# Kernel optimization log

Hardware: AMD Instinct MI355X
Metric: run time of the kernel (lower is better)

## Reference

```python
import jax, jax.numpy as jnp
import numpy as np

S, T, B, E, H, V = 64, 64, 64, 256, 256, 32000
PAD = 0


def _lstm_layer(X, Wih, Whh, b, h0, c0):
    # X: (time, B, in), torch gate order i,f,g,o
    def step(carry, x_t):
        h, c = carry
        z = x_t @ Wih.T + h @ Whh.T + b
        i, f, g, o = jnp.split(z, 4, axis=-1)
        c = jax.nn.sigmoid(f) * c + jax.nn.sigmoid(i) * jnp.tanh(g)
        h = jax.nn.sigmoid(o) * jnp.tanh(c)
        return (h, c), h
    (hT, cT), outs = jax.lax.scan(step, (h0, c0), X)
    return outs, hT, cT


def setup_inputs() -> dict:
    key = jax.random.key(0)
    ks = jax.random.split(key, 20)
    p = lambda k, shape: (jax.random.normal(k, shape, jnp.float32) * 0.05)
    inp = {
        "source_padded": jax.random.randint(ks[0], (S, B), 0, V, jnp.int32),
        "target_padded": jax.random.randint(ks[1], (T, B), 0, V, jnp.int32),
        "src_emb": p(ks[2], (V, E)),
        "tgt_emb": p(ks[3], (V, E)),
        "enc_Wih_f": p(ks[4], (4 * H, E)),
        "enc_Whh_f": p(ks[5], (4 * H, H)),
        "enc_b_f": p(ks[6], (4 * H,)),
        "enc_Wih_b": p(ks[7], (4 * H, E)),
        "enc_Whh_b": p(ks[8], (4 * H, H)),
        "enc_b_b": p(ks[9], (4 * H,)),
        "dec_Wih": p(ks[10], (4 * H, E + H)),
        "dec_Whh": p(ks[11], (4 * H, H)),
        "dec_b": p(ks[12], (4 * H,)),
        "Wh": p(ks[13], (H, 2 * H)),
        "Wc": p(ks[14], (H, 2 * H)),
        "Watt": p(ks[15], (H, 2 * H)),
        "Wcomb": p(ks[16], (H, 3 * H)),
        "Wvocab": p(ks[17], (V, H)),
    }
    return inp


def reference(source_padded, target_padded, src_emb, tgt_emb,
              enc_Wih_f, enc_Whh_f, enc_b_f, enc_Wih_b, enc_Whh_b, enc_b_b,
              dec_Wih, dec_Whh, dec_b, Wh, Wc, Watt, Wcomb, Wvocab):
    X = src_emb[source_padded]                      # (S,B,E)
    h0 = jnp.zeros((B, H), X.dtype)
    c0 = jnp.zeros((B, H), X.dtype)
    # bidirectional encoder (all sequences full length -> pack is identity)
    fwd_out, hf, cf = _lstm_layer(X, enc_Wih_f, enc_Whh_f, enc_b_f, h0, c0)
    bwd_out, hb, cb = _lstm_layer(X[::-1], enc_Wih_b, enc_Whh_b, enc_b_b, h0, c0)
    bwd_out = bwd_out[::-1]
    enc_hiddens = jnp.concatenate([fwd_out, bwd_out], -1).transpose(1, 0, 2)  # (B,S,2H)
    dec_h = jnp.concatenate([hf, hb], -1) @ Wh.T     # h_projection
    dec_c = jnp.concatenate([cf, cb], -1) @ Wc.T     # c_projection
    enc_proj = enc_hiddens @ Watt.T                  # (B,S,H)

    Y = tgt_emb[target_padded[:-1]]                  # (T-1,B,E)

    def dstep(carry, Y_t):
        h, c, o_prev = carry
        x = jnp.concatenate([Y_t, o_prev], -1)       # (B,E+H)
        z = x @ dec_Wih.T + h @ dec_Whh.T + dec_b
        i, f, g, o = jnp.split(z, 4, axis=-1)
        c = jax.nn.sigmoid(f) * c + jax.nn.sigmoid(i) * jnp.tanh(g)
        h = jax.nn.sigmoid(o) * jnp.tanh(c)
        e_t = jnp.einsum('bsh,bh->bs', enc_proj, h)  # attention scores
        alpha = jax.nn.softmax(e_t, axis=-1)         # no pads -> mask is no-op
        a_t = jnp.einsum('bs,bsd->bd', alpha, enc_hiddens)  # context (B,2H)
        O_t = jnp.tanh(jnp.concatenate([a_t, h], -1) @ Wcomb.T)  # dropout=eval
        return (h, c, O_t), O_t

    _, outs = jax.lax.scan(dstep, (dec_h, dec_c, jnp.zeros((B, H), X.dtype)), Y)
    P = jax.nn.log_softmax(outs @ Wvocab.T, axis=-1)          # (T-1,B,V)
    gold = jnp.take_along_axis(P, target_padded[1:][..., None], axis=-1)[..., 0]
    tmask = (target_padded[1:] != PAD).astype(P.dtype)
    return (gold * tmask).sum(axis=0)                          # (B,)
```

## Files before the change

kernel.cpp:

```cpp
#include <hip/hip_runtime.h>
#include <hip/hip_bf16.h>

static constexpr int S = 64, T = 64, B = 64, E = 256, H = 256, V = 32000;
static constexpr int H4 = 4 * H;
static constexpr int NCHUNK = 500;
static constexpr int NROW = (T - 1) * B;
static constexpr int LDP = 264;

typedef short bf16x8 __attribute__((ext_vector_type(8)));
typedef float f32x4 __attribute__((ext_vector_type(4)));
typedef unsigned long long ull;

__device__ __forceinline__ float sigf(float x) { return 1.0f / (1.0f + __expf(-x)); }
__device__ __forceinline__ float tanhfast(float x) { return 1.0f - 2.0f / (__expf(2.0f * x) + 1.0f); }
__device__ __forceinline__ float bflo(uint w) { return __uint_as_float(w << 16); }
__device__ __forceinline__ float bfhi(uint w) { return __uint_as_float(w & 0xffff0000u); }
__device__ __forceinline__ ushort f2bu(float x) {
  return __bfloat16_as_ushort(__float2bfloat16(x));
}

__device__ __forceinline__ void st_u32(uint* p, uint v) {
  __hip_atomic_store(p, v, __ATOMIC_RELAXED, __HIP_MEMORY_SCOPE_AGENT);
}
__device__ __forceinline__ uint ld_u32(const uint* p) {
  return __hip_atomic_load(p, __ATOMIC_RELAXED, __HIP_MEMORY_SCOPE_AGENT);
}

__global__ __launch_bounds__(256) void k_cvt_bf16(const float* __restrict__ src,
                                                  __hip_bfloat16* __restrict__ dst, int n) {
  int i = blockIdx.x * 256 + threadIdx.x;
  if (i < n) dst[i] = __float2bfloat16(src[i]);
}

__global__ __launch_bounds__(256) void k_cvt_slice(const float* __restrict__ src,
                                                   __hip_bfloat16* __restrict__ dst) {
  int n = blockIdx.x, tid = threadIdx.x;
  dst[n * 256 + tid] = __float2bfloat16(src[n * 512 + tid]);
}

__global__ __launch_bounds__(256) void k_gather(const int* __restrict__ idx,
                                                const float* __restrict__ emb,
                                                __hip_bfloat16* __restrict__ dst) {
  int r = blockIdx.x, tid = threadIdx.x;
  dst[r * 256 + tid] = __float2bfloat16(emb[idx[r] * E + tid]);
}

__global__ __launch_bounds__(256) void k_pack4(const float* __restrict__ src,
                                               uint2* __restrict__ dst,
                                               int total, int jshift, int ld, int off) {
  int idx = blockIdx.x * 256 + threadIdx.x;
  if (idx >= total) return;
  int J = 1 << jshift;
  int i = idx >> jshift, j = idx & (J - 1);
  const float* s = src + (size_t)j * ld + off + 4 * i;
  float4 v = *(const float4*)s;
  uint2 o;
  o.x = (uint)f2bu(v.x) | ((uint)f2bu(v.y) << 16);
  o.y = (uint)f2bu(v.z) | ((uint)f2bu(v.w) << 16);
  dst[(size_t)i * J + j] = o;
}

#define MFMA_TILE_BODY(Abase, Wbase, rb, cb)                                     \
  const int tid = threadIdx.x;                                                   \
  const int lane = tid & 63, wid = tid >> 6;                                     \
  const int wr = wid >> 1, wc = wid & 1;                                         \
  const int l15 = lane & 15, l4 = lane >> 4;                                     \
  for (int it = 0; it < 8; it++) {                                               \
    int c = it * 256 + tid;                                                      \
    int row = c >> 5, off = (c & 31) * 8;                                        \
    *(uint4*)&Asl[row * LDP + off] =                                             \
        *(const uint4*)((Abase) + (size_t)((rb) + row) * 256 + off);             \
    *(uint4*)&Bsl[row * LDP + off] =                                             \
        *(const uint4*)((Wbase) + (size_t)((cb) + row) * 256 + off);             \
  }                                                                              \
  __syncthreads();                                                               \
  f32x4 acc[2][2];                                                               \
  for (int m = 0; m < 2; m++)                                                    \
    for (int n = 0; n < 2; n++) acc[m][n] = (f32x4){0.f, 0.f, 0.f, 0.f};         \
  for (int kk = 0; kk < 8; kk++) {                                               \
    int ko = kk * 32 + l4 * 8;                                                   \
    bf16x8 a0 = *(const bf16x8*)&Asl[(wr * 32 + l15) * LDP + ko];                \
    bf16x8 a1 = *(const bf16x8*)&Asl[(wr * 32 + 16 + l15) * LDP + ko];           \
    bf16x8 b0 = *(const bf16x8*)&Bsl[(wc * 32 + l15) * LDP + ko];                \
    bf16x8 b1 = *(const bf16x8*)&Bsl[(wc * 32 + 16 + l15) * LDP + ko];           \
    acc[0][0] = __builtin_amdgcn_mfma_f32_16x16x32_bf16(a0, b0, acc[0][0], 0, 0, 0); \
    acc[0][1] = __builtin_amdgcn_mfma_f32_16x16x32_bf16(a0, b1, acc[0][1], 0, 0, 0); \
    acc[1][0] = __builtin_amdgcn_mfma_f32_16x16x32_bf16(a1, b0, acc[1][0], 0, 0, 0); \
    acc[1][1] = __builtin_amdgcn_mfma_f32_16x16x32_bf16(a1, b1, acc[1][1], 0, 0, 0); \
  }

__global__ __launch_bounds__(256) void k_gemm_bias(
    const __hip_bfloat16* __restrict__ A, const __hip_bfloat16* __restrict__ W,
    const float* __restrict__ bias, float* __restrict__ C, int ldc) {
  __shared__ __align__(16) ushort Asl[64 * LDP];
  __shared__ __align__(16) ushort Bsl[64 * LDP];
  const int cb = blockIdx.x * 64, rb = blockIdx.y * 64;
  MFMA_TILE_BODY((const ushort*)A, (const ushort*)W, rb, cb)
  #pragma unroll
  for (int m = 0; m < 2; m++)
    #pragma unroll
    for (int n = 0; n < 2; n++) {
      int col = cb + wc * 32 + n * 16 + l15;
      float bv = bias[col];
      #pragma unroll
      for (int r = 0; r < 4; r++) {
        int row = rb + wr * 32 + m * 16 + l4 * 4 + r;
        C[(size_t)row * ldc + col] = acc[m][n][r] + bv;
      }
    }
}

__global__ __launch_bounds__(256) void k_encproj_mfma(
    const __hip_bfloat16* __restrict__ fwd_bf, const __hip_bfloat16* __restrict__ bwd_bf,
    const __hip_bfloat16* __restrict__ Watt_bf, __hip_bfloat16* __restrict__ encproj_bf) {
  __shared__ __align__(16) ushort Asl[64 * LDP];
  __shared__ __align__(16) ushort Bsl[64 * LDP];
  const int cb = blockIdx.x * 64, rb = blockIdx.y * 64;
  const int tid = threadIdx.x;
  const int lane = tid & 63, wid = tid >> 6;
  const int wr = wid >> 1, wc = wid & 1;
  const int l15 = lane & 15, l4 = lane >> 4;
  f32x4 acc[2][2];
  #pragma unroll
  for (int m = 0; m < 2; m++)
    #pragma unroll
    for (int n = 0; n < 2; n++) acc[m][n] = (f32x4){0.f, 0.f, 0.f, 0.f};
  for (int kt = 0; kt < 2; kt++) {
    if (kt) __syncthreads();
    for (int it = 0; it < 8; it++) {
      int c = it * 256 + tid;
      int row = c >> 5, off = (c & 31) * 8;
      int r = rb + row, s = r >> 6, bb = r & 63;
      const ushort* arow = (kt == 0)
          ? (const ushort*)fwd_bf + (size_t)(s * 64 + bb) * 256
          : (const ushort*)bwd_bf + (size_t)(s * 64 + bb) * 256;
      *(uint4*)&Asl[row * LDP + off] = *(const uint4*)(arow + off);
      *(uint4*)&Bsl[row * LDP + off] =
          *(const uint4*)((const ushort*)Watt_bf + (size_t)(cb + row) * 512 + kt * 256 + off);
    }
    __syncthreads();
    for (int kk = 0; kk < 8; kk++) {
      int ko = kk * 32 + l4 * 8;
      bf16x8 a0 = *(const bf16x8*)&Asl[(wr * 32 + l15) * LDP + ko];
      bf16x8 a1 = *(const bf16x8*)&Asl[(wr * 32 + 16 + l15) * LDP + ko];
      bf16x8 b0 = *(const bf16x8*)&Bsl[(wc * 32 + l15) * LDP + ko];
      bf16x8 b1 = *(const bf16x8*)&Bsl[(wc * 32 + 16 + l15) * LDP + ko];
      acc[0][0] = __builtin_amdgcn_mfma_f32_16x16x32_bf16(a0, b0, acc[0][0], 0, 0, 0);
      acc[0][1] = __builtin_amdgcn_mfma_f32_16x16x32_bf16(a0, b1, acc[0][1], 0, 0, 0);
      acc[1][0] = __builtin_amdgcn_mfma_f32_16x16x32_bf16(a1, b0, acc[1][0], 0, 0, 0);
      acc[1][1] = __builtin_amdgcn_mfma_f32_16x16x32_bf16(a1, b1, acc[1][1], 0, 0, 0);
    }
  }
  #pragma unroll
  for (int m = 0; m < 2; m++)
    #pragma unroll
    for (int n = 0; n < 2; n++) {
      int col = cb + wc * 32 + n * 16 + l15;
      #pragma unroll
      for (int r = 0; r < 4; r++) {
        int row = rb + wr * 32 + m * 16 + l4 * 4 + r;
        int s = row >> 6, bb = row & 63;
        ((ushort*)encproj_bf)[(size_t)(bb * 64 + s) * 256 + col] = f2bu(acc[m][n][r]);
      }
    }
}

__global__ __launch_bounds__(256) void k_vocab2(
    const __hip_bfloat16* __restrict__ outs_bf, const __hip_bfloat16* __restrict__ Wv,
    const int* __restrict__ tgt, float* __restrict__ part_max,
    float* __restrict__ part_sum, float* __restrict__ gold) {
  __shared__ __align__(16) ushort Asl[64 * LDP];
  __shared__ __align__(16) ushort Bsl[64 * LDP];
  __shared__ int goldcol[64];
  __shared__ float pm[64][2], ps[64][2];
  const int vb = blockIdx.x;
  const int tid = threadIdx.x;
  const int lane = tid & 63, wid = tid >> 6;
  const int wr = wid >> 1, wc = wid & 1;
  const int l15 = lane & 15, l4 = lane >> 4;
  for (int it = 0; it < 8; it++) {
    int c = it * 256 + tid;
    int row = c >> 5, off = (c & 31) * 8;
    *(uint4*)&Bsl[row * LDP + off] =
        *(const uint4*)((const ushort*)Wv + (size_t)(vb * 64 + row) * 256 + off);
  }
  for (int t = 0; t < T - 1; t++) {
    __syncthreads();
    for (int it = 0; it < 8; it++) {
      int c = it * 256 + tid;
      int row = c >> 5, off = (c & 31) * 8;
      *(uint4*)&Asl[row * LDP + off] =
          *(const uint4*)((const ushort*)outs_bf + (size_t)(t * 64 + row) * 256 + off);
    }
    if (tid < 64) goldcol[tid] = tgt[(t + 1) * B + tid];
    __syncthreads();
    f32x4 acc[2][2];
    #pragma unroll
    for (int m = 0; m < 2; m++)
      #pragma unroll
      for (int n = 0; n < 2; n++) acc[m][n] = (f32x4){0.f, 0.f, 0.f, 0.f};
    for (int kk = 0; kk < 8; kk++) {
      int ko = kk * 32 + l4 * 8;
      bf16x8 a0 = *(const bf16x8*)&Asl[(wr * 32 + l15) * LDP + ko];
      bf16x8 a1 = *(const bf16x8*)&Asl[(wr * 32 + 16 + l15) * LDP + ko];
      bf16x8 b0 = *(const bf16x8*)&Bsl[(wc * 32 + l15) * LDP + ko];
      bf16x8 b1 = *(const bf16x8*)&Bsl[(wc * 32 + 16 + l15) * LDP + ko];
      acc[0][0] = __builtin_amdgcn_mfma_f32_16x16x32_bf16(a0, b0, acc[0][0], 0, 0, 0);
      acc[0][1] = __builtin_amdgcn_mfma_f32_16x16x32_bf16(a0, b1, acc[0][1], 0, 0, 0);
      acc[1][0] = __builtin_amdgcn_mfma_f32_16x16x32_bf16(a1, b0, acc[1][0], 0, 0, 0);
      acc[1][1] = __builtin_amdgcn_mfma_f32_16x16x32_bf16(a1, b1, acc[1][1], 0, 0, 0);
    }
    #pragma unroll
    for (int m = 0; m < 2; m++) {
      #pragma unroll
      for (int r = 0; r < 4; r++) {
        int row_local = wr * 32 + m * 16 + l4 * 4 + r;
        int gc = goldcol[row_local];
        #pragma unroll
        for (int n = 0; n < 2; n++) {
          int col = vb * 64 + wc * 32 + n * 16 + l15;
          if (col == gc) gold[t * 64 + row_local] = acc[m][n][r];
        }
        float v = fmaxf(acc[m][0][r], acc[m][1][r]);
        #pragma unroll
        for (int o = 1; o < 16; o <<= 1) v = fmaxf(v, __shfl_xor(v, o));
        float e = __expf(acc[m][0][r] - v) + __expf(acc[m][1][r] - v);
        #pragma unroll
        for (int o = 1; o < 16; o <<= 1) e += __shfl_xor(e, o);
        if (l15 == 0) { pm[row_local][wc] = v; ps[row_local][wc] = e; }
      }
    }
    __syncthreads();
    if (tid < 64) {
      float m0 = pm[tid][0], m1 = pm[tid][1];
      float M = fmaxf(m0, m1);
      float Ss = ps[tid][0] * __expf(m0 - M) + ps[tid][1] * __expf(m1 - M);
      part_max[(size_t)vb * NROW + t * 64 + tid] = M;
      part_sum[(size_t)vb * NROW + t * 64 + tid] = Ss;
    }
  }
}

__global__ __launch_bounds__(256) void k_enc4(
    const float* __restrict__ XwF, const float* __restrict__ XwB,
    const float* __restrict__ WhhF, const float* __restrict__ WhhB,
    uint* __restrict__ Xenc_u32,
    __hip_bfloat16* __restrict__ fwd_bf, __hip_bfloat16* __restrict__ bwd_bf,
    float* __restrict__ Cfin, uint* __restrict__ eflags) {
  __shared__ __align__(16) ushort Wl[128 * 264];
  __shared__ __align__(16) ushort Xa[16 * 264];
  __shared__ float zz[4][8][33];
  __shared__ float hsb[8][32];
  const int id = blockIdx.x;
  const int g = id & 7, kb = id >> 3;
  const int dir = kb >> 3, s = kb & 7;
  const int tid = threadIdx.x;
  const float* Whh = dir ? WhhB : WhhF;
  const float* Xw = dir ? XwB : XwF;
  uint* fl = eflags + (size_t)(g * 2 + dir) * 8 * 32;
  for (int i = tid; i < 128 * 256; i += 256) {
    int c = i >> 8, k2 = i & 255;
    int gate = c >> 5, jj = c & 31;
    Wl[c * 264 + k2] = f2bu(Whh[(size_t)(gate * 256 + s * 32 + jj) * 256 + k2]);
  }
  for (int i = tid; i < 16 * 264; i += 256) Xa[i] = 0;
  const int lane = tid & 63, w = tid >> 6;
  const int l15 = lane & 15, l4 = lane >> 4;
  const int tb = tid >> 5, tjj = tid & 31;
  float c_reg = 0.f;
  __syncthreads();
  for (int st = 0; st < 64; st++) {
    const int ts = dir ? 63 - st : st;
    const int par = st & 1;
    const uint* Xr = Xenc_u32 + (size_t)(par * 2 + dir) * 8192;
    uint* Xo = Xenc_u32 + (size_t)((par ^ 1) * 2 + dir) * 8192;
    for (int i = tid; i < 8 * 128; i += 256) {
      int row = i >> 7, colu = i & 127;
      uint v = ld_u32(Xr + (size_t)(8 * g + row) * 128 + colu);
      *(uint*)&Xa[row * 264 + colu * 2] = v;
    }
    __syncthreads();
    f32x4 a0v = (f32x4){0.f, 0.f, 0.f, 0.f}, a1v = (f32x4){0.f, 0.f, 0.f, 0.f};
    for (int kk = 0; kk < 8; kk++) {
      bf16x8 af = *(const bf16x8*)&Xa[l15 * 264 + kk * 32 + l4 * 8];
      bf16x8 b0 = *(const bf16x8*)&Wl[((2 * w) * 16 + l15) * 264 + kk * 32 + l4 * 8];
      bf16x8 b1 = *(const bf16x8*)&Wl[((2 * w + 1) * 16 + l15) * 264 + kk * 32 + l4 * 8];
      a0v = __builtin_amdgcn_mfma_f32_16x16x32_bf16(af, b0, a0v, 0, 0, 0);
      a1v = __builtin_amdgcn_mfma_f32_16x16x32_bf16(af, b1, a1v, 0, 0, 0);
    }
    if (l4 < 2) {
      #pragma unroll
      for (int r = 0; r < 4; r++) {
        int b = l4 * 4 + r;
        zz[w][b][l15] = a0v[r];
        zz[w][b][16 + l15] = a1v[r];
      }
    }
    __syncthreads();
    {
      int gb = 8 * g + tb, j = 32 * s + tjj;
      const float* xw = Xw + (size_t)(ts * 64 + gb) * 1024;
      float zi = zz[0][tb][tjj] + xw[j];
      float zf = zz[1][tb][tjj] + xw[256 + j];
      float zg = zz[2][tb][tjj] + xw[512 + j];
      float zo = zz[3][tb][tjj] + xw[768 + j];
      float c = sigf(zf) * c_reg + sigf(zi) * tanhfast(zg);
      c_reg = c;
      float h = sigf(zo) * tanhfast(c);
      hsb[tb][tjj] = h;
      ushort hb = f2bu(h);
      if (dir == 0) ((ushort*)fwd_bf)[(size_t)(st * 64 + gb) * 256 + j] = hb;
      else          ((ushort*)bwd_bf)[(size_t)((63 - st) * 64 + gb) * 256 + j] = hb;
    }
    __syncthreads();
    if (tid < 128) {
      int tb2 = tid >> 4, p = tid & 15;
      uint v = (uint)f2bu(hsb[tb2][2 * p]) | ((uint)f2bu(hsb[tb2][2 * p + 1]) << 16);
      st_u32(Xo + (size_t)(8 * g + tb2) * 128 + 16 * s + p, v);
    }
    __syncthreads();
    if (tid == 0) st_u32(&fl[s * 32], (uint)(st + 1));
    if (tid < 8)
      while (ld_u32(&fl[tid * 32]) < (uint)(st + 1)) __builtin_amdgcn_s_sleep(2);
    asm volatile("" ::: "memory");
    __syncthreads();
  }
  Cfin[(size_t)(dir * 64 + 8 * g + tb) * 256 + 32 * s + tjj] = c_reg;
}

__global__ __launch_bounds__(256) void k_dec_init3(
    const __hip_bfloat16* __restrict__ Xenc, const float* __restrict__ Cfin,
    const float* __restrict__ Wh, const float* __restrict__ Wc,
    uint* __restrict__ Xd_u32, float* __restrict__ decc0) {
  int b = blockIdx.x, tid = threadIdx.x;
  __shared__ __align__(16) float ch[512], cc[512];
  __shared__ float hh[256];
  ch[tid]       = __bfloat162float(Xenc[(size_t)(0 * 64 + b) * 256 + tid]);
  ch[256 + tid] = __bfloat162float(Xenc[(size_t)(1 * 64 + b) * 256 + tid]);
  cc[tid]       = Cfin[(size_t)(0 * 64 + b) * 256 + tid];
  cc[256 + tid] = Cfin[(size_t)(1 * 64 + b) * 256 + tid];
  __syncthreads();
  const float* wh = Wh + tid * 512;
  const float* wc = Wc + tid * 512;
  float ah = 0, ac = 0;
  for (int k = 0; k < 512; k += 4) {
    float4 hv = *(const float4*)&ch[k];
    float4 cv = *(const float4*)&cc[k];
    float4 w1 = *(const float4*)&wh[k];
    float4 w2 = *(const float4*)&wc[k];
    ah += hv.x * w1.x + hv.y * w1.y + hv.z * w1.z + hv.w * w1.w;
    ac += cv.x * w2.x + cv.y * w2.y + cv.z * w2.z + cv.w * w2.w;
  }
  decc0[b * 256 + tid] = ac;
  hh[tid] = ah;
  __syncthreads();
  if (tid < 128) {
    uint v = (uint)f2bu(hh[2 * tid]) | ((uint)f2bu(hh[2 * tid + 1]) << 16);
    Xd_u32[(size_t)b * 256 + tid] = v;
    Xd_u32[(size_t)b * 256 + 128 + tid] = 0u;
  }
}

__global__ __launch_bounds__(512) void k_dec5(
    const float* __restrict__ YW, const float* __restrict__ dWih,
    const float* __restrict__ dWhh, const uint2* __restrict__ Wcq,
    const __hip_bfloat16* __restrict__ encproj_bf,
    const __hip_bfloat16* __restrict__ fwd_bf, const __hip_bfloat16* __restrict__ bwd_bf,
    const float* __restrict__ decc0, uint* __restrict__ Xd_u32,
    __hip_bfloat16* __restrict__ outs_bf,
    uint* __restrict__ zflags, uint* __restrict__ aflags) {
  __shared__ __align__(16) char smem[155648];
  const int id = blockIdx.x;
  const int g = id & 7, kb = id >> 3;
  const int tid = threadIdx.x;
  uint* zfl = zflags + (size_t)g * 8 * 32;
  uint* afl = aflags + (size_t)g * 16 * 32;

  if (kb < 8) {
    const int s = kb;
    ushort* Wl = (ushort*)smem;
    ushort* Xa = (ushort*)(smem + 133120);
    float* zslds = (float*)(smem + 149760);
    float* hsb = (float*)(smem + 153856);
    for (int i = tid; i < 128 * 512; i += 512) {
      int c = i >> 9, k2 = i & 511;
      int gate = c >> 5, jj = c & 31;
      int gr = gate * 256 + 32 * s + jj;
      float v = (k2 < 256) ? dWhh[(size_t)gr * 256 + k2]
                           : dWih[(size_t)gr * 512 + 256 + (k2 - 256)];
      Wl[c * 520 + k2] = f2bu(v);
    }
    for (int i = tid; i < 16 * 520; i += 512) Xa[i] = 0;
    const int lane = tid & 63, w = tid >> 6;
    const int l15 = lane & 15, l4 = lane >> 4;
    float c_reg = 0.f;
    if (tid < 256) {
      int b = tid >> 5, jj = tid & 31;
      c_reg = decc0[(size_t)(8 * g + b) * 256 + 32 * s + jj];
    }
    __syncthreads();
    for (int t = 0; t < 63; t++) {
      if (t > 0) {
        if (tid < 8)
          while (ld_u32(&zfl[tid * 32]) < (uint)t) __builtin_amdgcn_s_sleep(2);
        else if (tid >= 64 && tid < 80)
          while (ld_u32(&afl[(tid - 64) * 32]) < (uint)t) __builtin_amdgcn_s_sleep(2);
        asm volatile("" ::: "memory");
        __syncthreads();
      }
      const uint* Xr = Xd_u32 + (size_t)(t & 1) * 16384;
      for (int i = tid; i < 8 * 256; i += 512) {
        int row = i >> 8, colu = i & 255;
        uint v = ld_u32(Xr + (size_t)(8 * g + row) * 256 + colu);
        *(uint*)&Xa[row * 520 + colu * 2] = v;
      }
      __syncthreads();
      f32x4 accv = (f32x4){0.f, 0.f, 0.f, 0.f};
      for (int kk = 0; kk < 16; kk++) {
        bf16x8 af = *(const bf16x8*)&Xa[l15 * 520 + kk * 32 + l4 * 8];
        bf16x8 bf = *(const bf16x8*)&Wl[(w * 16 + l15) * 520 + kk * 32 + l4 * 8];
        accv = __builtin_amdgcn_mfma_f32_16x16x32_bf16(af, bf, accv, 0, 0, 0);
      }
      if (l4 < 2) {
        #pragma unroll
        for (int r = 0; r < 4; r++) {
          int b = l4 * 4 + r;
          zslds[b * 128 + w * 16 + l15] = accv[r];
        }
      }
      __syncthreads();
      if (tid < 256) {
        int b = tid >> 5, jj = tid & 31;
        int gb = 8 * g + b;
        const float* yw = YW + (size_t)(t * 64 + gb) * 1024 + 32 * s + jj;
        float zi = zslds[b * 128 + jj] + yw[0];
        float zf = zslds[b * 128 + 32 + jj] + yw[256];
        float zg = zslds[b * 128 + 64 + jj] + yw[512];
        float zo = zslds[b * 128 + 96 + jj] + yw[768];
        float c = sigf(zf) * c_reg + sigf(zi) * tanhfast(zg);
        c_reg = c;
        hsb[b * 32 + jj] = sigf(zo) * tanhfast(c);
      }
      __syncthreads();
      if (tid < 128) {
        int b = tid >> 4, p = tid & 15;
        uint v = (uint)f2bu(hsb[b * 32 + 2 * p]) | ((uint)f2bu(hsb[b * 32 + 2 * p + 1]) << 16);
        st_u32(Xd_u32 + (size_t)((t & 1) ^ 1) * 16384 + (size_t)(8 * g + b) * 256 + 16 * s + p, v);
      }
      __syncthreads();
      if (tid == 0) st_u32(&zfl[s * 32], (uint)(t + 1));
    }
  } else {
    const int lb = (kb - 8) >> 1, jh = (kb - 8) & 1;
    const int b = 8 * g + lb;
    ushort* ep = (ushort*)smem;
    ushort* eh = (ushort*)(smem + 33792);
    float* hn = (float*)(smem + 100352);
    float* xcomb = (float*)(smem + 101376);
    float* e_l = (float*)(smem + 104448);
    float* alpha_l = (float*)(smem + 104704);
    float* op_l = (float*)(smem + 104960);
    float* Ost = (float*)(smem + 107008);
    for (int i = tid; i < 64 * 256; i += 512) {
      int s2 = i >> 8, k2 = i & 255;
      ep[s2 * 264 + k2] = ((const ushort*)encproj_bf)[(size_t)(b * 64 + s2) * 256 + k2];
    }
    for (int i = tid; i < 64 * 512; i += 512) {
      int s2 = i >> 9, d = i & 511;
      ushort v = (d < 256) ? ((const ushort*)fwd_bf)[(size_t)(s2 * 64 + b) * 256 + d]
                           : ((const ushort*)bwd_bf)[(size_t)(s2 * 64 + b) * 256 + d - 256];
      eh[s2 * 520 + d] = v;
    }
    __syncthreads();
    for (int t = 0; t < 63; t++) {
      if (tid < 8)
        while (ld_u32(&zfl[tid * 32]) < (uint)(t + 1)) __builtin_amdgcn_s_sleep(2);
      asm volatile("" ::: "memory");
      __syncthreads();
      if (tid < 128) {
        uint v = ld_u32(Xd_u32 + (size_t)((t & 1) ^ 1) * 16384 + (size_t)b * 256 + tid);
        hn[2 * tid] = bflo(v);
        hn[2 * tid + 1] = bfhi(v);
      }
      __syncthreads();
      {
        int s2 = tid >> 3, q8 = tid & 7;
        const ushort* pr = ep + s2 * 264 + q8 * 32;
        const float* hq = hn + q8 * 32;
        float a = 0.f;
        #pragma unroll 8
        for (int kk = 0; kk < 32; kk += 2) {
          uint wv = *(const uint*)(pr + kk);
          a += bflo(wv) * hq[kk] + bfhi(wv) * hq[kk + 1];
        }
        a += __shfl_xor(a, 1);
        a += __shfl_xor(a, 2);
        a += __shfl_xor(a, 4);
        if (q8 == 0) e_l[s2] = a;
      }
      __syncthreads();
      if (tid < 64) {
        float e = e_l[tid];
        float mx = e;
        #pragma unroll
        for (int o = 32; o > 0; o >>= 1) mx = fmaxf(mx, __shfl_xor(mx, o));
        float p = __expf(e - mx);
        float ss = p;
        #pragma unroll
        for (int o = 32; o > 0; o >>= 1) ss += __shfl_xor(ss, o);
        alpha_l[tid] = p / ss;
      }
      __syncthreads();
      {
        float a = 0.f;
        const ushort* col = eh + tid;
        #pragma unroll 8
        for (int s2 = 0; s2 < 64; s2++)
          a += alpha_l[s2] * __uint_as_float(((uint)col[s2 * 520]) << 16);
        xcomb[tid] = a;
        if (tid < 256) xcomb[512 + tid] = hn[tid];
      }
      __syncthreads();
      {
        int jl = tid & 127, kq = tid >> 7;
        int j = jh * 128 + jl;
        const uint2* wp = Wcq + (size_t)(kq * 48) * 256 + j;
        const float4* x4 = (const float4*)xcomb + kq * 48;
        float a = 0.f;
        #pragma unroll 6
        for (int ii = 0; ii < 48; ii++) {
          uint2 wv = wp[(size_t)ii * 256];
          float4 xv = x4[ii];
          a += bflo(wv.x) * xv.x + bfhi(wv.x) * xv.y + bflo(wv.y) * xv.z + bfhi(wv.y) * xv.w;
        }
        op_l[kq * 128 + jl] = a;
      }
      __syncthreads();
      if (tid < 128) {
        float sum = op_l[tid] + op_l[128 + tid] + op_l[256 + tid] + op_l[384 + tid];
        float O = tanhfast(sum);
        Ost[tid] = O;
        ((ushort*)outs_bf)[(size_t)(t * 64 + b) * 256 + jh * 128 + tid] = f2bu(O);
      }
      __syncthreads();
      if (tid < 64) {
        uint v = (uint)f2bu(Ost[2 * tid]) | ((uint)f2bu(Ost[2 * tid + 1]) << 16);
        st_u32(Xd_u32 + (size_t)((t & 1) ^ 1) * 16384 + (size_t)b * 256 + 128 + jh * 64 + tid, v);
      }
      __syncthreads();
      if (tid == 0) st_u32(&afl[(lb * 2 + jh) * 32], (uint)(t + 1));
    }
  }
}

__global__ __launch_bounds__(256) void k_final(
    const float* __restrict__ part_max, const float* __restrict__ part_sum,
    const float* __restrict__ gold, const int* __restrict__ tgt,
    float* __restrict__ out) {
  int b = blockIdx.x, tid = threadIdx.x;
  int tq = tid >> 2, q = tid & 3;
  __shared__ float lm[64][4], ls[64][4];
  __shared__ float red[64];
  if (tq < T - 1) {
    int n = tq * B + b;
    float m = -__builtin_inff(), s = 0;
    for (int i = q; i < NCHUNK; i += 4) {
      float pmv = part_max[(size_t)i * NROW + n];
      float psv = part_sum[(size_t)i * NROW + n];
      float M2 = fmaxf(m, pmv);
      s = s * __expf(m - M2) + psv * __expf(pmv - M2);
      m = M2;
    }
    lm[tq][q] = m;
    ls[tq][q] = s;
  }
  __syncthreads();
  if (tid < T - 1) {
    float M = fmaxf(fmaxf(lm[tid][0], lm[tid][1]), fmaxf(lm[tid][2], lm[tid][3]));
    float Ss = ls[tid][0] * __expf(lm[tid][0] - M) + ls[tid][1] * __expf(lm[tid][1] - M) +
               ls[tid][2] * __expf(lm[tid][2] - M) + ls[tid][3] * __expf(lm[tid][3] - M);
    float lse = M + logf(Ss);
    int g = tgt[(tid + 1) * B + b];
    red[tid] = (g != 0) ? (gold[tid * B + b] - lse) : 0.f;
  }
  if (tid == T - 1) red[T - 1] = 0.f;
  __syncthreads();
  if (tid == 0) {
    float s = 0;
    for (int i = 0; i < T - 1; i++) s += red[i];
    out[b] = s;
  }
}

extern "C" void kernel_launch(void* const* d_in, const int* in_sizes, int n_in,
                              void* d_out, int out_size, void* d_ws, size_t ws_size,
                              hipStream_t stream) {
  (void)in_sizes; (void)n_in; (void)out_size; (void)ws_size;
  const int*   src   = (const int*)  d_in[0];
  const int*   tgt   = (const int*)  d_in[1];
  const float* semb  = (const float*)d_in[2];
  const float* temb  = (const float*)d_in[3];
  const float* WihF  = (const float*)d_in[4];
  const float* WhhF  = (const float*)d_in[5];
  const float* bF    = (const float*)d_in[6];
  const float* WihB  = (const float*)d_in[7];
  const float* WhhB  = (const float*)d_in[8];
  const float* bB    = (const float*)d_in[9];
  const float* dWih  = (const float*)d_in[10];
  const float* dWhh  = (const float*)d_in[11];
  const float* db    = (const float*)d_in[12];
  const float* Wh    = (const float*)d_in[13];
  const float* Wc    = (const float*)d_in[14];
  const float* Watt  = (const float*)d_in[15];
  const float* Wcomb = (const float*)d_in[16];
  const float* Wv    = (const float*)d_in[17];
  float* out = (float*)d_out;

  char* wp = (char*)d_ws;
  auto alloc = [&](size_t bytes) -> char* {
    char* p = wp;
    wp += (bytes + 255) & ~(size_t)255;
    return p;
  };
  float* XwF  = (float*)alloc((size_t)S * B * H4 * 4);
  float* XwB  = (float*)alloc((size_t)S * B * H4 * 4);
  float* YW   = (float*)alloc((size_t)(T - 1) * B * H4 * 4);
  __hip_bfloat16* fwd_bf     = (__hip_bfloat16*)alloc((size_t)S * B * H * 2);
  __hip_bfloat16* bwd_bf     = (__hip_bfloat16*)alloc((size_t)S * B * H * 2);
  __hip_bfloat16* encproj_bf = (__hip_bfloat16*)alloc((size_t)B * S * H * 2);
  __hip_bfloat16* Ag         = (__hip_bfloat16*)alloc((size_t)S * B * E * 2);
  __hip_bfloat16* Yg         = (__hip_bfloat16*)alloc((size_t)(T - 1) * B * E * 2);
  __hip_bfloat16* WihF_bf    = (__hip_bfloat16*)alloc((size_t)H4 * E * 2);
  __hip_bfloat16* WihB_bf    = (__hip_bfloat16*)alloc((size_t)H4 * E * 2);
  __hip_bfloat16* dWih_bf    = (__hip_bfloat16*)alloc((size_t)H4 * E * 2);
  __hip_bfloat16* Wv_bf      = (__hip_bfloat16*)alloc((size_t)V * H * 2);
  __hip_bfloat16* Watt_bf    = (__hip_bfloat16*)alloc((size_t)H * 512 * 2);
  __hip_bfloat16* outs_bf    = (__hip_bfloat16*)alloc((size_t)NROW * H * 2);
  uint2* Wcq = (uint2*)alloc((size_t)192 * 256 * 8);
  float* part_max = (float*)alloc((size_t)NCHUNK * NROW * 4);
  float* part_sum = (float*)alloc((size_t)NCHUNK * NROW * 4);
  float* gold     = (float*)alloc((size_t)NROW * 4);
  float* Cfin  = (float*)alloc((size_t)2 * B * H * 4);
  float* decc0 = (float*)alloc((size_t)B * H * 4);
  __hip_bfloat16* Xenc = (__hip_bfloat16*)alloc((size_t)2 * 2 * B * H * 2);
  uint* Xdec = (uint*)alloc((size_t)2 * B * 256 * 4);
  char* stateBase = wp;
  uint* eflags = (uint*)alloc(16 * 8 * 32 * 4);
  uint* zflags = (uint*)alloc(8 * 8 * 32 * 4);
  uint* aflags = (uint*)alloc(8 * 16 * 32 * 4);
  size_t stateBytes = (size_t)(wp - stateBase);
  hipMemsetAsync(stateBase, 0, stateBytes, stream);
  hipMemsetAsync(Xenc, 0, (size_t)2 * 2 * B * H * 2, stream);

  hipLaunchKernelGGL(k_cvt_bf16, dim3((H4 * E + 255) / 256), dim3(256), 0, stream,
                     WihF, WihF_bf, H4 * E);
  hipLaunchKernelGGL(k_cvt_bf16, dim3((H4 * E + 255) / 256), dim3(256), 0, stream,
                     WihB, WihB_bf, H4 * E);
  hipLaunchKernelGGL(k_cvt_slice, dim3(H4), dim3(256), 0, stream, dWih, dWih_bf);
  hipLaunchKernelGGL(k_cvt_bf16, dim3((V * H + 255) / 256), dim3(256), 0, stream,
                     Wv, Wv_bf, V * H);
  hipLaunchKernelGGL(k_cvt_bf16, dim3((H * 512 + 255) / 256), dim3(256), 0, stream,
                     Watt, Watt_bf, H * 512);
  hipLaunchKernelGGL(k_gather, dim3(S * B), dim3(256), 0, stream, src, semb, Ag);
  hipLaunchKernelGGL(k_gather, dim3((T - 1) * B), dim3(256), 0, stream, tgt, temb, Yg);
  hipLaunchKernelGGL(k_pack4, dim3(192 * 256 / 256), dim3(256), 0, stream,
                     Wcomb, Wcq, 192 * 256, 8, 768, 0);

  hipLaunchKernelGGL(k_gemm_bias, dim3(H4 / 64, S * B / 64), dim3(256), 0, stream,
                     Ag, WihF_bf, bF, XwF, H4);
  hipLaunchKernelGGL(k_gemm_bias, dim3(H4 / 64, S * B / 64), dim3(256), 0, stream,
                     Ag, WihB_bf, bB, XwB, H4);
  hipLaunchKernelGGL(k_gemm_bias, dim3(H4 / 64, (T - 1) * B / 64), dim3(256), 0, stream,
                     Yg, dWih_bf, db, YW, H4);

  hipLaunchKernelGGL(k_enc4, dim3(128), dim3(256), 0, stream,
                     XwF, XwB, WhhF, WhhB, (uint*)Xenc, fwd_bf, bwd_bf, Cfin, eflags);
  hipLaunchKernelGGL(k_dec_init3, dim3(B), dim3(256), 0, stream,
                     Xenc, Cfin, Wh, Wc, Xdec, decc0);
  hipLaunchKernelGGL(k_encproj_mfma, dim3(4, 64), dim3(256), 0, stream,
                     fwd_bf, bwd_bf, Watt_bf, encproj_bf);

  hipLaunchKernelGGL(k_dec5, dim3(192), dim3(512), 0, stream,
                     YW, dWih, dWhh, Wcq, encproj_bf, fwd_bf, bwd_bf,
                     decc0, Xdec, outs_bf, zflags, aflags);

  hipLaunchKernelGGL(k_vocab2, dim3(NCHUNK), dim3(256), 0, stream,
                     outs_bf, Wv_bf, tgt, part_max, part_sum, gold);
  hipLaunchKernelGGL(k_final, dim3(B), dim3(256), 0, stream,
                     part_max, part_sum, gold, tgt, out);
}
```

Baseline: 1.253 ms.

## Split decoder recurrent matmul so h-part overlaps attention wait

The decoder's gate blocks now compute the h-dependent half of the recurrent MFMA (Whh·h) right after the new h is published, waiting only on the z-flags. The o_prev-dependent half (Wih·O_prev) is done after the attention flags arrive. This takes the Whh matmul off the critical path through the attention/combine blocks. The spin-wait sleep interval is also shortened, which adds some polling traffic in exchange for faster wakeups.

```diff
diff --git a/kernel.cpp b/kernel.cpp
--- a/kernel.cpp
+++ b/kernel.cpp
@@ -361,7 +361,7 @@
   }
 }
 
-__global__ __launch_bounds__(512) void k_dec5(
+__global__ __launch_bounds__(512) void k_dec6(
     const float* __restrict__ YW, const float* __restrict__ dWih,
     const float* __restrict__ dWhh, const uint2* __restrict__ Wcq,
     const __hip_bfloat16* __restrict__ encproj_bf,
@@ -399,24 +399,33 @@
       c_reg = decc0[(size_t)(8 * g + b) * 256 + 32 * s + jj];
     }
     __syncthreads();
+    for (int i = tid; i < 8 * 128; i += 512) {
+      int row = i >> 7, p = i & 127;
+      uint v = ld_u32(Xd_u32 + (size_t)(8 * g + row) * 256 + p);
+      *(uint*)&Xa[row * 520 + 2 * p] = v;
+    }
+    __syncthreads();
+    f32x4 accv = (f32x4){0.f, 0.f, 0.f, 0.f};
+    for (int kk = 0; kk < 8; kk++) {
+      bf16x8 af = *(const bf16x8*)&Xa[l15 * 520 + kk * 32 + l4 * 8];
+      bf16x8 bf = *(const bf16x8*)&Wl[(w * 16 + l15) * 520 + kk * 32 + l4 * 8];
+      accv = __builtin_amdgcn_mfma_f32_16x16x32_bf16(af, bf, accv, 0, 0, 0);
+    }
     for (int t = 0; t < 63; t++) {
+      const int par = t & 1;
       if (t > 0) {
-        if (tid < 8)
-          while (ld_u32(&zfl[tid * 32]) < (uint)t) __builtin_amdgcn_s_sleep(2);
-        else if (tid >= 64 && tid < 80)
-          while (ld_u32(&afl[(tid - 64) * 32]) < (uint)t) __builtin_amdgcn_s_sleep(2);
+        if (tid < 16)
+          while (ld_u32(&afl[tid * 32]) < (uint)t) __builtin_amdgcn_s_sleep(1);
         asm volatile("" ::: "memory");
         __syncthreads();
       }
-      const uint* Xr = Xd_u32 + (size_t)(t & 1) * 16384;
-      for (int i = tid; i < 8 * 256; i += 512) {
-        int row = i >> 8, colu = i & 255;
-        uint v = ld_u32(Xr + (size_t)(8 * g + row) * 256 + colu);
-        *(uint*)&Xa[row * 520 + colu * 2] = v;
-      }
-      __syncthreads();
-      f32x4 accv = (f32x4){0.f, 0.f, 0.f, 0.f};
-      for (int kk = 0; kk < 16; kk++) {
+      for (int i = tid; i < 8 * 128; i += 512) {
+        int row = i >> 7, p = i & 127;
+        uint v = ld_u32(Xd_u32 + (size_t)par * 16384 + (size_t)(8 * g + row) * 256 + 128 + p);
+        *(uint*)&Xa[row * 520 + 256 + 2 * p] = v;
+      }
+      __syncthreads();
+      for (int kk = 8; kk < 16; kk++) {
         bf16x8 af = *(const bf16x8*)&Xa[l15 * 520 + kk * 32 + l4 * 8];
         bf16x8 bf = *(const bf16x8*)&Wl[(w * 16 + l15) * 520 + kk * 32 + l4 * 8];
         accv = __builtin_amdgcn_mfma_f32_16x16x32_bf16(af, bf, accv, 0, 0, 0);
@@ -445,10 +454,28 @@
       if (tid < 128) {
         int b = tid >> 4, p = tid & 15;
         uint v = (uint)f2bu(hsb[b * 32 + 2 * p]) | ((uint)f2bu(hsb[b * 32 + 2 * p + 1]) << 16);
-        st_u32(Xd_u32 + (size_t)((t & 1) ^ 1) * 16384 + (size_t)(8 * g + b) * 256 + 16 * s + p, v);
+        st_u32(Xd_u32 + (size_t)(par ^ 1) * 16384 + (size_t)(8 * g + b) * 256 + 16 * s + p, v);
       }
       __syncthreads();
       if (tid == 0) st_u32(&zfl[s * 32], (uint)(t + 1));
+      if (t < 62) {
+        if (tid < 8)
+          while (ld_u32(&zfl[tid * 32]) < (uint)(t + 1)) __builtin_amdgcn_s_sleep(1);
+        asm volatile("" ::: "memory");
+        __syncthreads();
+        for (int i = tid; i < 8 * 128; i += 512) {
+          int row = i >> 7, p = i & 127;
+          uint v = ld_u32(Xd_u32 + (size_t)(par ^ 1) * 16384 + (size_t)(8 * g + row) * 256 + p);
+          *(uint*)&Xa[row * 520 + 2 * p] = v;
+        }
+        __syncthreads();
+        accv = (f32x4){0.f, 0.f, 0.f, 0.f};
+        for (int kk = 0; kk < 8; kk++) {
+          bf16x8 af = *(const bf16x8*)&Xa[l15 * 520 + kk * 32 + l4 * 8];
+          bf16x8 bf = *(const bf16x8*)&Wl[(w * 16 + l15) * 520 + kk * 32 + l4 * 8];
+          accv = __builtin_amdgcn_mfma_f32_16x16x32_bf16(af, bf, accv, 0, 0, 0);
+        }
+      }
     }
   } else {
     const int lb = (kb - 8) >> 1, jh = (kb - 8) & 1;
@@ -474,7 +501,7 @@
     __syncthreads();
     for (int t = 0; t < 63; t++) {
       if (tid < 8)
-        while (ld_u32(&zfl[tid * 32]) < (uint)(t + 1)) __builtin_amdgcn_s_sleep(2);
+        while (ld_u32(&zfl[tid * 32]) < (uint)(t + 1)) __builtin_amdgcn_s_sleep(1);
       asm volatile("" ::: "memory");
       __syncthreads();
       if (tid < 128) {
@@ -680,7 +707,7 @@
   hipLaunchKernelGGL(k_encproj_mfma, dim3(4, 64), dim3(256), 0, stream,
                      fwd_bf, bwd_bf, Watt_bf, encproj_bf);
 
-  hipLaunchKernelGGL(k_dec5, dim3(192), dim3(512), 0, stream,
+  hipLaunchKernelGGL(k_dec6, dim3(192), dim3(512), 0, stream,
                      YW, dWih, dWhh, Wcq, encproj_bf, fwd_bf, bwd_bf,
                      decc0, Xdec, outs_bf, zflags, aflags);
 
```

After: 1.209 ms. 1.04x faster.
